# Kernel tuning notes

Hardware: AMD Instinct MI355X
Metric: run time of the kernel (lower is better)

The kernel has to match this reference:

```python
import jax, jax.numpy as jnp
import numpy as np
import math

D_EMB = 1024
N_HEADS = 16
SCALE = 0.02
B, T = 4, 2048


def _norm(x):
    # torch.std_mean default: unbiased std (ddof=1) over last dim
    m = jnp.mean(x, axis=-1, keepdims=True)
    s = jnp.std(x, axis=-1, keepdims=True, ddof=1)
    return (x - m) / (s + 1e-05)


def setup_inputs() -> dict:
    key = jax.random.key(0)
    kx, kw = jax.random.split(key)
    x = jax.random.normal(kx, (B, D_EMB, T), dtype=jnp.float32)
    qkv = jax.random.normal(kw, (3, N_HEADS, D_EMB, D_EMB // N_HEADS), dtype=jnp.float32) * SCALE
    return {"x": x, "qkv": qkv}


def reference(x, qkv):
    Bsz, D, Tlen = x.shape
    H = qkv.shape[1]
    # (3, B, H, T, d_head)
    h = jnp.einsum('bdt,nhde->nbhte', x, qkv)
    q, k, v = h[0], h[1], h[2]
    q = _norm(q)
    k = _norm(k)
    scale = math.sqrt(D // H)  # torch: sqrt(d_emb // H)
    attn = jnp.einsum('bhte,bhse->bhts', q, k) / scale  # [B,H,T,T]
    attn = jax.nn.softmax(attn, axis=-1)
    out = jnp.einsum('bhts,bhse->bhet', attn, v)  # [B,H,d_head,T]
    return out.reshape(Bsz, D, Tlen)
```

## Files before the change

kernel.cpp:

```cpp
#include <hip/hip_runtime.h>
#include <hip/hip_bf16.h>

#define B_SZ 4
#define NHEADS 16
#define T_SZ 2048
#define DE 1024
#define DH 64
#define BH (B_SZ*NHEADS)
#define SCL 0.18033688011112042f
#define PSTR 88

typedef __attribute__((ext_vector_type(8))) short short8;
typedef __attribute__((ext_vector_type(4))) float float4v;
typedef __attribute__((ext_vector_type(2))) unsigned int uint2v;

__device__ __forceinline__ short f2bf(float f) {
    __hip_bfloat16 h = __float2bfloat16(f);
    return *reinterpret_cast<short*>(&h);
}
__device__ __forceinline__ unsigned int pack_bf2(float a, float b) {
    float2 f; f.x = a; f.y = b;
    __hip_bfloat162 h = __float22bfloat162_rn(f);
    return *reinterpret_cast<unsigned int*>(&h);
}
__device__ __forceinline__ float4v zero4() {
    float4v z = {0.f, 0.f, 0.f, 0.f};
    return z;
}
__device__ __forceinline__ int swz(int row, int g) {
    return row * 64 + (((g) ^ (row & 7)) << 3);
}
__device__ __forceinline__ void gl_lds16(const short* g, short* l) {
    __builtin_amdgcn_global_load_lds(
        (const __attribute__((address_space(1))) void*)g,
        (__attribute__((address_space(3))) void*)l, 16, 0, 0);
}

__global__ __launch_bounds__(256) void transpose_k(const float* __restrict__ src,
                                                   short* __restrict__ dst,
                                                   int R, int C) {
    __shared__ __align__(16) short tile[64 * 65];
    int c0 = blockIdx.x * 64, r0 = blockIdx.y * 64;
    src += (size_t)blockIdx.z * R * C;
    dst += (size_t)blockIdx.z * R * C;
    int tid = threadIdx.x;
#pragma unroll
    for (int it = 0; it < 16; ++it) {
        int idx = it * 256 + tid;
        int rr = idx >> 6, cc = idx & 63;
        tile[cc * 65 + rr] = f2bf(src[(size_t)(r0 + rr) * C + c0 + cc]);
    }
    __syncthreads();
#pragma unroll
    for (int it = 0; it < 16; ++it) {
        int idx = it * 256 + tid;
        int cc = idx >> 6, rr = idx & 63;
        dst[(size_t)(c0 + cc) * R + r0 + rr] = tile[cc * 65 + rr];
    }
}

__global__ __launch_bounds__(256, 2) void qkv_k(const short* __restrict__ XT,
                                                const short* __restrict__ WT,
                                                short* __restrict__ Qw,
                                                short* __restrict__ Kw,
                                                short* __restrict__ Vt) {
    __shared__ __align__(16) short ldsA[2][128 * 64];
    __shared__ __align__(16) short ldsB[2][128 * 64];
    int b  = blockIdx.x >> 4;
    int t0 = (blockIdx.x & 15) * 128;
    int n  = blockIdx.y >> 3;
    int h0 = (blockIdx.y & 7) * 2;
    int tid = threadIdx.x, wave = tid >> 6, lane = tid & 63;
    int l15 = lane & 15, quad = lane >> 4;
    int wr = wave >> 1, wc = wave & 1;

    const short* Arow = XT + ((size_t)b * T_SZ + t0) * DE;
    const short* Brow = WT + ((size_t)n * 1024 + h0 * 64) * DE;

    int rA = lane >> 3;
    int gl = (lane & 7) ^ rA;

    float4v acc[4][4];
#pragma unroll
    for (int mm = 0; mm < 4; ++mm)
#pragma unroll
        for (int j = 0; j < 4; ++j) acc[mm][j] = zero4();

    auto STAGE = [&](short* La, short* Lb, int k0) {
#pragma unroll
        for (int it = 0; it < 4; ++it) {
            int rowbase = it * 32 + wave * 8;
            gl_lds16(&Arow[(size_t)(rowbase + rA) * DE + k0 + gl * 8],
                     &La[(it * 256 + wave * 64) * 8]);
            gl_lds16(&Brow[(size_t)(rowbase + rA) * DE + k0 + gl * 8],
                     &Lb[(it * 256 + wave * 64) * 8]);
        }
    };
    auto COMPUTE = [&](const short* La, const short* Lb) {
#pragma unroll
        for (int ks = 0; ks < 2; ++ks) {
            short8 af[4], bf[4];
#pragma unroll
            for (int mm = 0; mm < 4; ++mm)
                af[mm] = *(const short8*)&La[swz(64 * wr + 16 * mm + l15, 4 * ks + quad)];
#pragma unroll
            for (int j = 0; j < 4; ++j)
                bf[j] = *(const short8*)&Lb[swz(64 * wc + 16 * j + l15, 4 * ks + quad)];
#pragma unroll
            for (int mm = 0; mm < 4; ++mm)
#pragma unroll
                for (int j = 0; j < 4; ++j)
                    acc[mm][j] = __builtin_amdgcn_mfma_f32_16x16x32_bf16(af[mm], bf[j], acc[mm][j], 0, 0, 0);
        }
    };

    STAGE(ldsA[0], ldsB[0], 0);
    __syncthreads();
    for (int k0 = 0; k0 < DE; k0 += 128) {
        STAGE(ldsA[1], ldsB[1], k0 + 64);
        COMPUTE(ldsA[0], ldsB[0]);
        __syncthreads();
        if (k0 + 128 < DE)
            STAGE(ldsA[0], ldsB[0], k0 + 128);
        COMPUTE(ldsA[1], ldsB[1]);
        __syncthreads();
    }

    int h = h0 + wc;
    int bh = b * NHEADS + h;
#pragma unroll
    for (int mm = 0; mm < 4; ++mm) {
        int tbase = t0 + 64 * wr + 16 * mm;
        if (n < 2) {
            float oscale = (n == 0) ? SCL : 1.0f;
            float mu[4], inv[4];
#pragma unroll
            for (int r = 0; r < 4; ++r) {
                float s1 = 0.f, s2 = 0.f;
#pragma unroll
                for (int jj = 0; jj < 4; ++jj) {
                    float v = acc[mm][jj][r];
                    s1 += v; s2 += v * v;
                }
                for (int sh = 1; sh < 16; sh <<= 1) {
                    s1 += __shfl_xor(s1, sh, 64);
                    s2 += __shfl_xor(s2, sh, 64);
                }
                mu[r] = s1 * (1.0f / 64.0f);
                float var = (s2 - 64.0f * mu[r] * mu[r]) * (1.0f / 63.0f);
                var = fmaxf(var, 0.0f);
                inv[r] = oscale / (sqrtf(var) + 1e-5f);
            }
            short* dst = (n == 0 ? Qw : Kw) + (size_t)bh * T_SZ * DH;
#pragma unroll
            for (int r = 0; r < 4; ++r) {
                int t = tbase + quad * 4 + r;
#pragma unroll
                for (int jj = 0; jj < 4; ++jj) {
                    float v = (acc[mm][jj][r] - mu[r]) * inv[r];
                    dst[(size_t)t * DH + 16 * jj + l15] = f2bf(v);
                }
            }
        } else {
#pragma unroll
            for (int r = 0; r < 4; ++r) {
                int t = tbase + quad * 4 + r;
#pragma unroll
                for (int jj = 0; jj < 4; ++jj) {
                    Vt[((size_t)bh * DH + 16 * jj + l15) * T_SZ + t] =
                        f2bf(acc[mm][jj][r]);
                }
            }
        }
    }
}

__global__ __launch_bounds__(256, 4) void attn_k(const short* __restrict__ Qw,
                                                 const short* __restrict__ Kw,
                                                 const short* __restrict__ Vt,
                                                 float* __restrict__ out) {
    __shared__ __align__(16) char smem[38912];
    short* ldsK = (short*)smem;
    short* ldsV = (short*)(smem + 8192);
    short* ldsP = (short*)(smem + 16384);
    float* ldsO = (float*)smem;

    int bh = blockIdx.x;
    int t0 = blockIdx.y * 128;
    int b = bh >> 4, h = bh & 15;
    int tid = threadIdx.x, wave = tid >> 6, lane = tid & 63;
    int l15 = lane & 15, quad = lane >> 4;
    int tw = t0 + 32 * wave;

    const short* Qp = Qw + (size_t)bh * T_SZ * DH;
    const short* Kp = Kw + (size_t)bh * T_SZ * DH;
    const short* Vp = Vt + (size_t)bh * DH * T_SZ;
    short* Pw = ldsP + wave * 32 * PSTR;

    int rA = lane >> 3;
    int g8 = lane & 7;

    short8 qf[2][2];
#pragma unroll
    for (int tt = 0; tt < 2; ++tt)
#pragma unroll
        for (int ks = 0; ks < 2; ++ks)
            qf[tt][ks] = *(const short8*)&Qp[(size_t)(tw + 16 * tt + l15) * DH + ks * 32 + quad * 8];

    const short one_bf = (short)0x3F80;
    short8 ones = {one_bf, one_bf, one_bf, one_bf, one_bf, one_bf, one_bf, one_bf};

    float4v o[2][4];
    float4v ol[2];
#pragma unroll
    for (int tt = 0; tt < 2; ++tt) {
        ol[tt] = zero4();
#pragma unroll
        for (int j = 0; j < 4; ++j) o[tt][j] = zero4();
    }

    short8 rk[2], rv[2];
    auto LOADNEXT = [&](int s) {
#pragma unroll
        for (int it = 0; it < 2; ++it) {
            int rowbase = it * 32 + wave * 8;
            rk[it] = *(const short8*)&Kp[(size_t)(s + rowbase + rA) * DH + g8 * 8];
            rv[it] = *(const short8*)&Vp[(size_t)(rowbase + rA) * T_SZ + s + g8 * 8];
        }
    };
    auto WRITESTAGE = [&]() {
#pragma unroll
        for (int it = 0; it < 2; ++it) {
            int rowbase = it * 32 + wave * 8;
            *(short8*)&ldsK[swz(rowbase + rA, g8)] = rk[it];
            *(short8*)&ldsV[swz(rowbase + rA, g8)] = rv[it];
        }
    };

    LOADNEXT(0);
    WRITESTAGE();
    __syncthreads();

    for (int s0 = 0; s0 < T_SZ; s0 += 64) {
        int sn = (s0 + 64 < T_SZ) ? s0 + 64 : 0;
        LOADNEXT(sn);

#pragma unroll
        for (int j = 0; j < 4; ++j) {
            short8 k0 = *(const short8*)&ldsK[swz(16 * j + l15, quad)];
            short8 k1 = *(const short8*)&ldsK[swz(16 * j + l15, 4 + quad)];
#pragma unroll
            for (int tt = 0; tt < 2; ++tt) {
                float4v z = zero4();
                z = __builtin_amdgcn_mfma_f32_16x16x32_bf16(k0, qf[tt][0], z, 0, 0, 0);
                z = __builtin_amdgcn_mfma_f32_16x16x32_bf16(k1, qf[tt][1], z, 0, 0, 0);
                float p0 = __builtin_amdgcn_exp2f(z[0]);
                float p1 = __builtin_amdgcn_exp2f(z[1]);
                float p2 = __builtin_amdgcn_exp2f(z[2]);
                float p3 = __builtin_amdgcn_exp2f(z[3]);
                uint2v u = { pack_bf2(p0, p1), pack_bf2(p2, p3) };
                *(uint2v*)&Pw[(16 * tt + l15) * PSTR + 16 * j + quad * 4] = u;
            }
        }

        short8 pf[2][2];
#pragma unroll
        for (int tt = 0; tt < 2; ++tt) {
            pf[tt][0] = *(const short8*)&Pw[(16 * tt + l15) * PSTR + quad * 8];
            pf[tt][1] = *(const short8*)&Pw[(16 * tt + l15) * PSTR + 32 + quad * 8];
            ol[tt] = __builtin_amdgcn_mfma_f32_16x16x32_bf16(pf[tt][0], ones, ol[tt], 0, 0, 0);
            ol[tt] = __builtin_amdgcn_mfma_f32_16x16x32_bf16(pf[tt][1], ones, ol[tt], 0, 0, 0);
        }
#pragma unroll
        for (int j = 0; j < 4; ++j) {
            short8 v0 = *(const short8*)&ldsV[swz(16 * j + l15, quad)];
            short8 v1 = *(const short8*)&ldsV[swz(16 * j + l15, 4 + quad)];
#pragma unroll
            for (int tt = 0; tt < 2; ++tt) {
                o[tt][j] = __builtin_amdgcn_mfma_f32_16x16x32_bf16(pf[tt][0], v0, o[tt][j], 0, 0, 0);
                o[tt][j] = __builtin_amdgcn_mfma_f32_16x16x32_bf16(pf[tt][1], v1, o[tt][j], 0, 0, 0);
            }
        }

        __syncthreads();
        WRITESTAGE();
        __syncthreads();
    }

    float4v rinv[2];
#pragma unroll
    for (int tt = 0; tt < 2; ++tt)
#pragma unroll
        for (int r = 0; r < 4; ++r)
            rinv[tt][r] = 1.0f / ol[tt][r];

#pragma unroll
    for (int ph = 0; ph < 2; ++ph) {
        __syncthreads();
        if ((wave >> 1) == ph) {
            float* Ow = ldsO + (wave & 1) * (64 * 36);
#pragma unroll
            for (int tt = 0; tt < 2; ++tt)
#pragma unroll
                for (int j = 0; j < 4; ++j) {
                    float4v ov = o[tt][j] * rinv[tt];
                    *(float4v*)&Ow[(16 * j + l15) * 36 + 16 * tt + quad * 4] = ov;
                }
        }
        __syncthreads();
#pragma unroll
        for (int it = 0; it < 4; ++it) {
            int idx = it * 256 + tid;
            int rg = idx >> 9;
            int rid = idx & 511;
            int e = rid >> 3, t4 = (rid & 7) * 4;
            *(float4v*)&out[((size_t)(b * DE + h * DH + e)) * T_SZ + t0 + 32 * (2 * ph + rg) + t4] =
                *(const float4v*)&ldsO[rg * (64 * 36) + e * 36 + t4];
        }
    }
}

extern "C" void kernel_launch(void* const* d_in, const int* in_sizes, int n_in,
                              void* d_out, int out_size, void* d_ws, size_t ws_size,
                              hipStream_t stream) {
    const float* x = (const float*)d_in[0];
    const float* w = (const float*)d_in[1];
    float* out = (float*)d_out;
    char* ws = (char*)d_ws;

    const size_t XT_BYTES = (size_t)B_SZ * T_SZ * DE * 2;
    const size_t WT_BYTES = (size_t)3 * NHEADS * DH * DE * 2;
    const size_t QKV_BYTES = (size_t)BH * T_SZ * DH * 2;

    short* XT = (short*)(ws);
    short* WT = (short*)(ws + XT_BYTES);
    short* Qw = (short*)(ws + XT_BYTES + WT_BYTES);
    short* Kw = (short*)(ws + XT_BYTES + WT_BYTES + QKV_BYTES);
    short* Vt = (short*)(ws + XT_BYTES + WT_BYTES + 2 * QKV_BYTES);

    transpose_k<<<dim3(T_SZ / 64, DE / 64, B_SZ), 256, 0, stream>>>(x, XT, DE, T_SZ);
    transpose_k<<<dim3(1, DE / 64, 3 * NHEADS), 256, 0, stream>>>(w, WT, DE, DH);
    qkv_k<<<dim3(64, 24), 256, 0, stream>>>(XT, WT, Qw, Kw, Vt);
    attn_k<<<dim3(BH, T_SZ / 128), 256, 0, stream>>>(Qw, Kw, Vt, out);
}
```

Before: 243.7 us.

## Rewrite attention with 32x32 MFMA, register-resident P, and double-buffered K/V

The attention kernel moves from 16x16x32 to 32x32x16 bf16 MFMA tiles, and each wave now covers 64 query rows. The probability tile stays in registers and is rearranged with v_permlane32_swap instead of round-tripping through LDS. Row sums are accumulated with scalar adds instead of a ones-vector MFMA. K/V staging is double-buffered, so each iteration needs one barrier instead of two. Output is written straight from registers rather than through an LDS transpose. In exchange, register pressure rises (launch bounds drop to 2 blocks per CU), there are half as many blocks, and the global stores may coalesce less well.

```diff
diff --git a/kernel.cpp b/kernel.cpp
--- a/kernel.cpp
+++ b/kernel.cpp
@@ -8,11 +8,12 @@
 #define DH 64
 #define BH (B_SZ*NHEADS)
 #define SCL 0.18033688011112042f
-#define PSTR 88
 
 typedef __attribute__((ext_vector_type(8))) short short8;
 typedef __attribute__((ext_vector_type(4))) float float4v;
+typedef __attribute__((ext_vector_type(16))) float f32x16;
 typedef __attribute__((ext_vector_type(2))) unsigned int uint2v;
+typedef __attribute__((ext_vector_type(4))) unsigned int uint4v;
 
 __device__ __forceinline__ short f2bf(float f) {
     __hip_bfloat16 h = __float2bfloat16(f);
@@ -175,147 +176,148 @@
     }
 }
 
-__global__ __launch_bounds__(256, 4) void attn_k(const short* __restrict__ Qw,
+__global__ __launch_bounds__(256, 2) void attn_k(const short* __restrict__ Qw,
                                                  const short* __restrict__ Kw,
                                                  const short* __restrict__ Vt,
                                                  float* __restrict__ out) {
-    __shared__ __align__(16) char smem[38912];
+    __shared__ __align__(16) char smem[32768];
     short* ldsK = (short*)smem;
-    short* ldsV = (short*)(smem + 8192);
-    short* ldsP = (short*)(smem + 16384);
-    float* ldsO = (float*)smem;
+    short* ldsV = (short*)(smem + 16384);
+    float* ldsL = (float*)smem;
 
     int bh = blockIdx.x;
-    int t0 = blockIdx.y * 128;
+    int t0 = blockIdx.y * 256;
     int b = bh >> 4, h = bh & 15;
     int tid = threadIdx.x, wave = tid >> 6, lane = tid & 63;
-    int l15 = lane & 15, quad = lane >> 4;
-    int tw = t0 + 32 * wave;
+    int l31 = lane & 31, b5 = lane >> 5;
+    int tw = t0 + 64 * wave;
 
     const short* Qp = Qw + (size_t)bh * T_SZ * DH;
     const short* Kp = Kw + (size_t)bh * T_SZ * DH;
     const short* Vp = Vt + (size_t)bh * DH * T_SZ;
-    short* Pw = ldsP + wave * 32 * PSTR;
 
     int rA = lane >> 3;
     int g8 = lane & 7;
 
-    short8 qf[2][2];
+    short8 qf[2][4];
 #pragma unroll
     for (int tt = 0; tt < 2; ++tt)
 #pragma unroll
-        for (int ks = 0; ks < 2; ++ks)
-            qf[tt][ks] = *(const short8*)&Qp[(size_t)(tw + 16 * tt + l15) * DH + ks * 32 + quad * 8];
-
-    const short one_bf = (short)0x3F80;
-    short8 ones = {one_bf, one_bf, one_bf, one_bf, one_bf, one_bf, one_bf, one_bf};
-
-    float4v o[2][4];
-    float4v ol[2];
-#pragma unroll
-    for (int tt = 0; tt < 2; ++tt) {
-        ol[tt] = zero4();
-#pragma unroll
-        for (int j = 0; j < 4; ++j) o[tt][j] = zero4();
-    }
+        for (int kk = 0; kk < 4; ++kk)
+            qf[tt][kk] = *(const short8*)&Qp[(size_t)(tw + 32 * tt + l31) * DH + 16 * kk + 8 * b5];
+
+    f32x16 o[2][2];
+    float ol[2] = {0.f, 0.f};
+#pragma unroll
+    for (int tt = 0; tt < 2; ++tt)
+#pragma unroll
+        for (int et = 0; et < 2; ++et) o[tt][et] = (f32x16)0.0f;
 
     short8 rk[2], rv[2];
     auto LOADNEXT = [&](int s) {
 #pragma unroll
         for (int it = 0; it < 2; ++it) {
-            int rowbase = it * 32 + wave * 8;
-            rk[it] = *(const short8*)&Kp[(size_t)(s + rowbase + rA) * DH + g8 * 8];
-            rv[it] = *(const short8*)&Vp[(size_t)(rowbase + rA) * T_SZ + s + g8 * 8];
+            int row = 16 * wave + 8 * it + rA;
+            rk[it] = *(const short8*)&Kp[(size_t)(s + row) * DH + g8 * 8];
+            rv[it] = *(const short8*)&Vp[(size_t)row * T_SZ + s + g8 * 8];
         }
     };
-    auto WRITESTAGE = [&]() {
+    auto WRITESTAGE = [&](int buf) {
+        short* Kb = ldsK + buf * 4096;
+        short* Vb = ldsV + buf * 4096;
 #pragma unroll
         for (int it = 0; it < 2; ++it) {
-            int rowbase = it * 32 + wave * 8;
-            *(short8*)&ldsK[swz(rowbase + rA, g8)] = rk[it];
-            *(short8*)&ldsV[swz(rowbase + rA, g8)] = rv[it];
+            int row = 16 * wave + 8 * it + rA;
+            *(short8*)&Kb[swz(row, g8)] = rk[it];
+            *(short8*)&Vb[swz(row, g8)] = rv[it];
         }
     };
 
     LOADNEXT(0);
-    WRITESTAGE();
+    WRITESTAGE(0);
     __syncthreads();
 
     for (int s0 = 0; s0 < T_SZ; s0 += 64) {
-        int sn = (s0 + 64 < T_SZ) ? s0 + 64 : 0;
-        LOADNEXT(sn);
-
-#pragma unroll
-        for (int j = 0; j < 4; ++j) {
-            short8 k0 = *(const short8*)&ldsK[swz(16 * j + l15, quad)];
-            short8 k1 = *(const short8*)&ldsK[swz(16 * j + l15, 4 + quad)];
-#pragma unroll
-            for (int tt = 0; tt < 2; ++tt) {
-                float4v z = zero4();
-                z = __builtin_amdgcn_mfma_f32_16x16x32_bf16(k0, qf[tt][0], z, 0, 0, 0);
-                z = __builtin_amdgcn_mfma_f32_16x16x32_bf16(k1, qf[tt][1], z, 0, 0, 0);
-                float p0 = __builtin_amdgcn_exp2f(z[0]);
-                float p1 = __builtin_amdgcn_exp2f(z[1]);
-                float p2 = __builtin_amdgcn_exp2f(z[2]);
-                float p3 = __builtin_amdgcn_exp2f(z[3]);
-                uint2v u = { pack_bf2(p0, p1), pack_bf2(p2, p3) };
-                *(uint2v*)&Pw[(16 * tt + l15) * PSTR + 16 * j + quad * 4] = u;
-            }
-        }
-
-        short8 pf[2][2];
+        int cur = (s0 >> 6) & 1;
+        LOADNEXT((s0 + 64) & (T_SZ - 1));
+        const short* Kc = ldsK + cur * 4096;
+        const short* Vc = ldsV + cur * 4096;
+
+        short8 af[2][4];
+#pragma unroll
+        for (int ss = 0; ss < 2; ++ss)
+#pragma unroll
+            for (int kk = 0; kk < 4; ++kk)
+                af[ss][kk] = *(const short8*)&Kc[swz(32 * ss + l31, 2 * kk + b5)];
+
+        uint2v u[2][2][4];
 #pragma unroll
         for (int tt = 0; tt < 2; ++tt) {
-            pf[tt][0] = *(const short8*)&Pw[(16 * tt + l15) * PSTR + quad * 8];
-            pf[tt][1] = *(const short8*)&Pw[(16 * tt + l15) * PSTR + 32 + quad * 8];
-            ol[tt] = __builtin_amdgcn_mfma_f32_16x16x32_bf16(pf[tt][0], ones, ol[tt], 0, 0, 0);
-            ol[tt] = __builtin_amdgcn_mfma_f32_16x16x32_bf16(pf[tt][1], ones, ol[tt], 0, 0, 0);
-        }
-#pragma unroll
-        for (int j = 0; j < 4; ++j) {
-            short8 v0 = *(const short8*)&ldsV[swz(16 * j + l15, quad)];
-            short8 v1 = *(const short8*)&ldsV[swz(16 * j + l15, 4 + quad)];
-#pragma unroll
-            for (int tt = 0; tt < 2; ++tt) {
-                o[tt][j] = __builtin_amdgcn_mfma_f32_16x16x32_bf16(pf[tt][0], v0, o[tt][j], 0, 0, 0);
-                o[tt][j] = __builtin_amdgcn_mfma_f32_16x16x32_bf16(pf[tt][1], v1, o[tt][j], 0, 0, 0);
-            }
-        }
-
+#pragma unroll
+            for (int ss = 0; ss < 2; ++ss) {
+                f32x16 z = (f32x16)0.0f;
+#pragma unroll
+                for (int kk = 0; kk < 4; ++kk)
+                    z = __builtin_amdgcn_mfma_f32_32x32x16_bf16(af[ss][kk], qf[tt][kk], z, 0, 0, 0);
+#pragma unroll
+                for (int g = 0; g < 4; ++g) {
+                    float p0 = __builtin_amdgcn_exp2f(z[4 * g + 0]);
+                    float p1 = __builtin_amdgcn_exp2f(z[4 * g + 1]);
+                    float p2 = __builtin_amdgcn_exp2f(z[4 * g + 2]);
+                    float p3 = __builtin_amdgcn_exp2f(z[4 * g + 3]);
+                    ol[tt] += (p0 + p1) + (p2 + p3);
+                    u[tt][ss][g].x = pack_bf2(p0, p1);
+                    u[tt][ss][g].y = pack_bf2(p2, p3);
+                }
+            }
+        }
+
+        short8 vf[2][4];
+#pragma unroll
+        for (int et = 0; et < 2; ++et)
+#pragma unroll
+            for (int kk = 0; kk < 4; ++kk)
+                vf[et][kk] = *(const short8*)&Vc[swz(32 * et + l31, 2 * kk + b5)];
+
+#pragma unroll
+        for (int tt = 0; tt < 2; ++tt) {
+#pragma unroll
+            for (int kks = 0; kks < 4; ++kks) {
+                const int ssb = kks >> 1, ga = 2 * (kks & 1);
+                unsigned a0 = u[tt][ssb][ga].x,     a1 = u[tt][ssb][ga].y;
+                unsigned b0 = u[tt][ssb][ga + 1].x, b1 = u[tt][ssb][ga + 1].y;
+                asm("v_permlane32_swap_b32 %0, %1" : "+v"(a0), "+v"(b0));
+                asm("v_permlane32_swap_b32 %0, %1" : "+v"(a1), "+v"(b1));
+                uint4v up; up.x = a0; up.y = a1; up.z = b0; up.w = b1;
+                short8 pf = *(short8*)&up;
+                o[tt][0] = __builtin_amdgcn_mfma_f32_32x32x16_bf16(pf, vf[0][kks], o[tt][0], 0, 0, 0);
+                o[tt][1] = __builtin_amdgcn_mfma_f32_32x32x16_bf16(pf, vf[1][kks], o[tt][1], 0, 0, 0);
+            }
+        }
+
+        WRITESTAGE(cur ^ 1);
         __syncthreads();
-        WRITESTAGE();
-        __syncthreads();
-    }
-
-    float4v rinv[2];
-#pragma unroll
-    for (int tt = 0; tt < 2; ++tt)
-#pragma unroll
-        for (int r = 0; r < 4; ++r)
-            rinv[tt][r] = 1.0f / ol[tt][r];
-
-#pragma unroll
-    for (int ph = 0; ph < 2; ++ph) {
-        __syncthreads();
-        if ((wave >> 1) == ph) {
-            float* Ow = ldsO + (wave & 1) * (64 * 36);
-#pragma unroll
-            for (int tt = 0; tt < 2; ++tt)
-#pragma unroll
-                for (int j = 0; j < 4; ++j) {
-                    float4v ov = o[tt][j] * rinv[tt];
-                    *(float4v*)&Ow[(16 * j + l15) * 36 + 16 * tt + quad * 4] = ov;
-                }
-        }
-        __syncthreads();
-#pragma unroll
-        for (int it = 0; it < 4; ++it) {
-            int idx = it * 256 + tid;
-            int rg = idx >> 9;
-            int rid = idx & 511;
-            int e = rid >> 3, t4 = (rid & 7) * 4;
-            *(float4v*)&out[((size_t)(b * DE + h * DH + e)) * T_SZ + t0 + 32 * (2 * ph + rg) + t4] =
-                *(const float4v*)&ldsO[rg * (64 * 36) + e * 36 + t4];
+    }
+
+#pragma unroll
+    for (int tt = 0; tt < 2; ++tt) {
+        float l = ol[tt] + __shfl_xor(ol[tt], 32, 64);
+        if (lane < 32) ldsL[wave * 64 + tt * 32 + lane] = 1.0f / l;
+    }
+
+#pragma unroll
+    for (int tt = 0; tt < 2; ++tt) {
+#pragma unroll
+        for (int g = 0; g < 4; ++g) {
+            float4v ri = *(const float4v*)&ldsL[wave * 64 + tt * 32 + 8 * g + 4 * b5];
+#pragma unroll
+            for (int et = 0; et < 2; ++et) {
+                float4v ov;
+#pragma unroll
+                for (int i = 0; i < 4; ++i) ov[i] = o[tt][et][4 * g + i] * ri[i];
+                *(float4v*)&out[(size_t)(b * DE + h * DH + 32 * et + l31) * T_SZ
+                                + tw + 32 * tt + 8 * g + 4 * b5] = ov;
+            }
         }
     }
 }
@@ -341,5 +343,5 @@
     transpose_k<<<dim3(T_SZ / 64, DE / 64, B_SZ), 256, 0, stream>>>(x, XT, DE, T_SZ);
     transpose_k<<<dim3(1, DE / 64, 3 * NHEADS), 256, 0, stream>>>(w, WT, DE, DH);
     qkv_k<<<dim3(64, 24), 256, 0, stream>>>(XT, WT, Qw, Kw, Vt);
-    attn_k<<<dim3(BH, T_SZ / 128), 256, 0, stream>>>(Qw, Kw, Vt, out);
-}
+    attn_k<<<dim3(BH, T_SZ / 256), 256, 0, stream>>>(Qw, Kw, Vt, out);
+}
```

Result: faster. 237.4 us (-2.6%).
